# Kernel tuning notes

Measured on AMD Instinct MI355X. Metric: run time of the kernel, lower is better.

## Reference

```python
import jax, jax.numpy as jnp
import numpy as np

HIDDEN_DIM = 512
RADIUS = 128


def rel_pos_indexes(seq_len_q: int, seq_len_k: int, radius: int):
    # (i - j) clamped to [-radius, radius], shifted to [0, 2*radius]
    i = jnp.arange(seq_len_k)[None, :]   # [1, Sk]
    j = jnp.arange(seq_len_q)[:, None]   # [Sq, 1]
    return jnp.clip(i - j, -radius, radius) + radius  # [Sq, Sk] int


def setup_inputs() -> dict:
    key = jax.random.key(0)
    kq, kk, kv, ke = jax.random.split(key, 4)
    B, Sq, Sk, d = 4, 2048, 2048, HIDDEN_DIM
    Q = jax.random.normal(kq, (B, Sq, d), dtype=jnp.float32)
    K = jax.random.normal(kk, (B, Sk, d), dtype=jnp.float32)
    V = jax.random.normal(kv, (B, Sk, d), dtype=jnp.float32)
    # learned relative-position embedding table: (2R+1, d)
    rel_embeds = jax.random.normal(ke, (2 * RADIUS + 1, d), dtype=jnp.float32)
    return {"Q": Q, "K": K, "V": V, "rel_embeds": rel_embeds}


def reference(Q, K, V, rel_embeds):
    B, Sq, d = Q.shape
    Sk = K.shape[1]
    normalizer = jnp.asarray(d ** 0.5, dtype=Q.dtype)
    # content scores: [B, Sq, Sk]
    energy = jnp.einsum('bqd,bkd->bqk', Q, K)
    # relative scores: Q against the (2R+1) relative embeddings -> [B, Sq, 2R+1]
    Q_rel = jnp.einsum('bqd,rd->bqr', Q, rel_embeds)
    idx = rel_pos_indexes(Sq, Sk, RADIUS)  # [Sq, Sk]
    # gather along last dim per query row (same index map for every batch)
    rel_shift = jnp.take_along_axis(Q_rel, idx[None, :, :].repeat(B, axis=0), axis=2)
    energy = (energy + rel_shift) / normalizer
    attn = jax.nn.softmax(energy, axis=2)
    Z = jnp.einsum('bqk,bkd->bqd', attn, V)
    return attn, Z
```

## Files before the change

### kernel.cpp

```cpp
#include <hip/hip_runtime.h>

#define BATCH 4
#define SQL 2048
#define SKL 2048
#define DIM 512
#define NR 257
#define NRP 288
#define RAD 128

typedef __bf16 bf16x8 __attribute__((ext_vector_type(8)));
typedef float f32x4 __attribute__((ext_vector_type(4)));
typedef unsigned short u16;
typedef u16 u16x4 __attribute__((ext_vector_type(4)));
typedef u16 u16x8 __attribute__((ext_vector_type(8)));

__device__ inline u16 f2bf(float x) {
  union { float f; unsigned u; } v; v.f = x;
  unsigned r = v.u + 0x7FFF + ((v.u >> 16) & 1);
  return (u16)(r >> 16);
}

__device__ inline void glds16(const u16* g, const u16* l) {
  __builtin_amdgcn_global_load_lds(
      (const __attribute__((address_space(1))) void*)g,
      (__attribute__((address_space(3))) void*)l, 16, 0, 0);
}


__global__ void cvt_kernel(const f32x4* __restrict__ src, u16x4* __restrict__ dst, int n4) {
  int i = blockIdx.x * 256 + threadIdx.x;
  if (i >= n4) return;
  f32x4 f = src[i];
  u16x4 o;
#pragma unroll
  for (int e = 0; e < 4; e++) o[e] = f2bf(f[e]);
  dst[i] = o;
}

__global__ void cvt_rel_kernel(const float* __restrict__ rel, u16* __restrict__ relb) {
  int i = blockIdx.x * 256 + threadIdx.x;
  int r = i >> 9;
  relb[i] = (r < NR) ? f2bf(rel[i]) : (u16)0;
}

__global__ void transpose_v_kernel(const float* __restrict__ V, u16* __restrict__ Vt) {
  __shared__ float tile[32][33];
  int b = blockIdx.z;
  int k0 = blockIdx.x * 32, d0 = blockIdx.y * 32;
  int tx = threadIdx.x, ty = threadIdx.y;
#pragma unroll
  for (int r = 0; r < 4; r++)
    tile[ty + r * 8][tx] = V[((long)b * SKL + k0 + ty + r * 8) * DIM + d0 + tx];
  __syncthreads();
#pragma unroll
  for (int r = 0; r < 4; r++)
    Vt[((long)b * DIM + d0 + ty + r * 8) * SKL + k0 + tx] = f2bf(tile[tx][ty + r * 8]);
}

__global__ __launch_bounds__(256) void qrel_kernel(const u16* __restrict__ Qb,
                                                   const u16* __restrict__ relb,
                                                   float* __restrict__ Qrel) {
  int tid = threadIdx.x;
  int wave = tid >> 6, lane = tid & 63;
  int m0 = blockIdx.x * 64 + wave * 16;
  int j0 = blockIdx.y * 2;
  int fr = lane & 15, fk = (lane >> 4) * 8;
  f32x4 acc[2] = {};
  const u16* qrow = Qb + (long)(m0 + fr) * DIM + fk;
  const u16* r0 = relb + (long)(j0 * 16 + fr) * DIM + fk;
  const u16* r1 = r0 + 16 * DIM;
  for (int k0 = 0; k0 < DIM; k0 += 32) {
    bf16x8 a = *(const bf16x8*)(qrow + k0);
    bf16x8 b0 = *(const bf16x8*)(r0 + k0);
    bf16x8 b1 = *(const bf16x8*)(r1 + k0);
    acc[0] = __builtin_amdgcn_mfma_f32_16x16x32_bf16(a, b0, acc[0], 0, 0, 0);
    acc[1] = __builtin_amdgcn_mfma_f32_16x16x32_bf16(a, b1, acc[1], 0, 0, 0);
  }
  int cr = (lane >> 4) * 4, cc = lane & 15;
#pragma unroll
  for (int t = 0; t < 2; t++)
#pragma unroll
    for (int r = 0; r < 4; r++)
      Qrel[(long)(m0 + cr + r) * NRP + (j0 + t) * 16 + cc] = acc[t][r];
}

__global__ __launch_bounds__(256) void energy_kernel(const u16* __restrict__ Qb,
                                                     const u16* __restrict__ Kb,
                                                     const float* __restrict__ Qrel,
                                                     u16* __restrict__ S) {
  int b = blockIdx.z;
  int m0 = blockIdx.y * 128;
  int n0 = blockIdx.x * 128;
  const u16* A = Qb + (long)b * SQL * DIM;
  const u16* Bp = Kb + (long)b * SKL * DIM;
  __shared__ u16 As[128 * 32];
  __shared__ u16 Bs[128 * 32];
  int tid = threadIdx.x;
  int wave = tid >> 6, lane = tid & 63;
  int wm = (wave >> 1) * 64, wn = (wave & 1) * 64;
  int fr = lane & 15, fk = (lane >> 4) * 8;
  int srow = wave * 32 + (lane >> 2);
  int scol = (lane & 3) * 8;
  f32x4 acc[4][4] = {};
  for (int k0 = 0; k0 < DIM; k0 += 32) {
    __syncthreads();
    glds16(A + (long)(m0 + srow) * DIM + k0 + scol, As + (wave * 2 + 0) * 512);
    glds16(A + (long)(m0 + srow + 16) * DIM + k0 + scol, As + (wave * 2 + 1) * 512);
    glds16(Bp + (long)(n0 + srow) * DIM + k0 + scol, Bs + (wave * 2 + 0) * 512);
    glds16(Bp + (long)(n0 + srow + 16) * DIM + k0 + scol, Bs + (wave * 2 + 1) * 512);
    __syncthreads();
    bf16x8 af[4], bfr[4];
#pragma unroll
    for (int i = 0; i < 4; i++) af[i] = *(const bf16x8*)(As + (wm + i * 16 + fr) * 32 + fk);
#pragma unroll
    for (int j = 0; j < 4; j++) bfr[j] = *(const bf16x8*)(Bs + (wn + j * 16 + fr) * 32 + fk);
#pragma unroll
    for (int i = 0; i < 4; i++)
#pragma unroll
      for (int j = 0; j < 4; j++)
        acc[i][j] = __builtin_amdgcn_mfma_f32_16x16x32_bf16(af[i], bfr[j], acc[i][j], 0, 0, 0);
  }
  const float inv_norm = 0.04419417382415922f;
  int cr = (lane >> 4) * 4, cc = lane & 15;
#pragma unroll
  for (int i = 0; i < 4; i++) {
#pragma unroll
    for (int r = 0; r < 4; r++) {
      int q = m0 + wm + i * 16 + cr + r;
      const float* qrow = Qrel + ((long)b * SQL + q) * NRP;
      u16* sr = S + ((long)b * SQL + q) * SKL;
#pragma unroll
      for (int j = 0; j < 4; j++) {
        int k = n0 + wn + j * 16 + cc;
        int dlt = k - q;
        dlt = dlt < -RAD ? -RAD : (dlt > RAD ? RAD : dlt);
        sr[k] = f2bf((acc[i][j][r] + qrow[dlt + RAD]) * inv_norm);
      }
    }
  }
}

__global__ __launch_bounds__(256) void softmax_kernel(u16* __restrict__ S,
                                                      float* __restrict__ attn) {
  long row = blockIdx.x;
  u16* srow = S + row * SKL;
  float* arow = attn + row * SKL;
  int tid = threadIdx.x;
  int wave = tid >> 6, lane = tid & 63;
  bf16x8 v = *(const bf16x8*)(srow + tid * 8);
  float f[8];
#pragma unroll
  for (int e = 0; e < 8; e++) f[e] = (float)v[e];
  float m = -1e30f;
#pragma unroll
  for (int e = 0; e < 8; e++) m = fmaxf(m, f[e]);
  for (int o = 32; o > 0; o >>= 1) m = fmaxf(m, __shfl_xor(m, o));
  __shared__ float red[4];
  if (lane == 0) red[wave] = m;
  __syncthreads();
  m = fmaxf(fmaxf(red[0], red[1]), fmaxf(red[2], red[3]));
  __syncthreads();
  float s = 0.0f;
  float e8[8];
#pragma unroll
  for (int e = 0; e < 8; e++) { e8[e] = __expf(f[e] - m); s += e8[e]; }
  for (int o = 32; o > 0; o >>= 1) s += __shfl_xor(s, o);
  if (lane == 0) red[wave] = s;
  __syncthreads();
  s = red[0] + red[1] + red[2] + red[3];
  float inv = 1.0f / s;
  f32x4 o0, o1;
  u16x8 pb;
#pragma unroll
  for (int e = 0; e < 4; e++) {
    float p = e8[e] * inv;
    o0[e] = p; pb[e] = f2bf(p);
  }
#pragma unroll
  for (int e = 0; e < 4; e++) {
    float p = e8[e + 4] * inv;
    o1[e] = p; pb[e + 4] = f2bf(p);
  }
  *(f32x4*)(arow + tid * 8) = o0;
  *(f32x4*)(arow + tid * 8 + 4) = o1;
  *(u16x8*)(srow + tid * 8) = pb;
}

__global__ __launch_bounds__(256) void z_kernel(const u16* __restrict__ S,
                                                const u16* __restrict__ Vt,
                                                float* __restrict__ Z) {
  int b = blockIdx.z;
  int m0 = blockIdx.y * 64;
  int n0 = blockIdx.x * 128;
  const u16* A = S + (long)b * SQL * SKL;
  const u16* Bp = Vt + (long)b * DIM * SKL;
  __shared__ u16 As[64 * 32];
  __shared__ u16 Bs[128 * 32];
  int tid = threadIdx.x;
  int wave = tid >> 6, lane = tid & 63;
  int wm = (wave >> 1) * 32, wn = (wave & 1) * 64;
  int fr = lane & 15, fk = (lane >> 4) * 8;
  int srowA = wave * 16 + (lane >> 2);
  int srowB = wave * 32 + (lane >> 2);
  int scol = (lane & 3) * 8;
  f32x4 acc[2][4] = {};
  for (int k0 = 0; k0 < SKL; k0 += 32) {
    __syncthreads();
    glds16(A + (long)(m0 + srowA) * SKL + k0 + scol, As + wave * 512);
    glds16(Bp + (long)(n0 + srowB) * SKL + k0 + scol, Bs + (wave * 2 + 0) * 512);
    glds16(Bp + (long)(n0 + srowB + 16) * SKL + k0 + scol, Bs + (wave * 2 + 1) * 512);
    __syncthreads();
    bf16x8 af[2], bfr[4];
#pragma unroll
    for (int i = 0; i < 2; i++) af[i] = *(const bf16x8*)(As + (wm + i * 16 + fr) * 32 + fk);
#pragma unroll
    for (int j = 0; j < 4; j++) bfr[j] = *(const bf16x8*)(Bs + (wn + j * 16 + fr) * 32 + fk);
#pragma unroll
    for (int i = 0; i < 2; i++)
#pragma unroll
      for (int j = 0; j < 4; j++)
        acc[i][j] = __builtin_amdgcn_mfma_f32_16x16x32_bf16(af[i], bfr[j], acc[i][j], 0, 0, 0);
  }
  int cr = (lane >> 4) * 4, cc = lane & 15;
#pragma unroll
  for (int i = 0; i < 2; i++)
#pragma unroll
    for (int r = 0; r < 4; r++) {
      int q = m0 + wm + i * 16 + cr + r;
      float* zrow = Z + ((long)b * SQL + q) * DIM;
#pragma unroll
      for (int j = 0; j < 4; j++)
        zrow[n0 + wn + j * 16 + cc] = acc[i][j][r];
    }
}


extern "C" void kernel_launch(void* const* d_in, const int* in_sizes, int n_in,
                              void* d_out, int out_size, void* d_ws, size_t ws_size,
                              hipStream_t stream) {
  const float* Q = (const float*)d_in[0];
  const float* K = (const float*)d_in[1];
  const float* V = (const float*)d_in[2];
  const float* rel = (const float*)d_in[3];
  float* attn = (float*)d_out;
  float* Z = attn + (long)BATCH * SQL * SKL;

  char* ws = (char*)d_ws;
  u16* Qb   = (u16*)ws;
  u16* Kb   = (u16*)(ws + 8388608);
  u16* Vt   = (u16*)(ws + 16777216);
  u16* relb = (u16*)(ws + 25165824);
  float* Qrel = (float*)(ws + 25460736);
  u16* S    = (u16*)(ws + 34897920);

  cvt_kernel<<<4096, 256, 0, stream>>>((const f32x4*)Q, (u16x4*)Qb, 1048576);
  cvt_kernel<<<4096, 256, 0, stream>>>((const f32x4*)K, (u16x4*)Kb, 1048576);
  cvt_rel_kernel<<<576, 256, 0, stream>>>(rel, relb);
  transpose_v_kernel<<<dim3(64, 16, BATCH), dim3(32, 8), 0, stream>>>(V, Vt);
  qrel_kernel<<<dim3(128, 9), 256, 0, stream>>>(Qb, relb, Qrel);
  energy_kernel<<<dim3(16, 16, BATCH), 256, 0, stream>>>(Qb, Kb, Qrel, S);
  softmax_kernel<<<8192, 256, 0, stream>>>(S, attn);
  z_kernel<<<dim3(4, 32, BATCH), 256, 0, stream>>>(S, Vt, Z);
}
```

Measured before the change: 248.7 us.

## Fuse prep kernels and move relative-position bias add into softmax

Merges the Q/K conversion, V transpose, rel-embedding conversion and Q·rel GEMM into a single prep kernel, with the GEMM reading fp32 inputs directly. The relative bias gather moves out of the energy GEMM epilogue into the softmax kernel, which stages the row's scaled Qrel in LDS. This cuts launch overhead and the scattered global gathers in the energy epilogue, at the cost of a larger heterogeneous prep kernel and extra LDS work in softmax.

```diff
diff --git a/kernel.cpp b/kernel.cpp
--- a/kernel.cpp
+++ b/kernel.cpp
@@ -20,73 +20,86 @@
   return (u16)(r >> 16);
 }
 
+__device__ inline bf16x8 cvt8m(f32x4 lo, f32x4 hi, float m) {
+  u16x8 o;
+#pragma unroll
+  for (int e = 0; e < 4; e++) o[e] = f2bf(lo[e] * m);
+#pragma unroll
+  for (int e = 0; e < 4; e++) o[e + 4] = f2bf(hi[e] * m);
+  union { u16x8 u; bf16x8 b; } c; c.u = o; return c.b;
+}
+
 __device__ inline void glds16(const u16* g, const u16* l) {
   __builtin_amdgcn_global_load_lds(
       (const __attribute__((address_space(1))) void*)g,
       (__attribute__((address_space(3))) void*)l, 16, 0, 0);
 }
 
-
-__global__ void cvt_kernel(const f32x4* __restrict__ src, u16x4* __restrict__ dst, int n4) {
-  int i = blockIdx.x * 256 + threadIdx.x;
-  if (i >= n4) return;
-  f32x4 f = src[i];
-  u16x4 o;
-#pragma unroll
-  for (int e = 0; e < 4; e++) o[e] = f2bf(f[e]);
-  dst[i] = o;
-}
-
-__global__ void cvt_rel_kernel(const float* __restrict__ rel, u16* __restrict__ relb) {
-  int i = blockIdx.x * 256 + threadIdx.x;
-  int r = i >> 9;
-  relb[i] = (r < NR) ? f2bf(rel[i]) : (u16)0;
-}
-
-__global__ void transpose_v_kernel(const float* __restrict__ V, u16* __restrict__ Vt) {
+__global__ __launch_bounds__(256) void prep_kernel(const float* __restrict__ Q,
+                                                   const float* __restrict__ K,
+                                                   const float* __restrict__ V,
+                                                   const float* __restrict__ rel,
+                                                   u16x4* __restrict__ Qb,
+                                                   u16x4* __restrict__ Kb,
+                                                   u16* __restrict__ Vt,
+                                                   float* __restrict__ Qrel) {
   __shared__ float tile[32][33];
-  int b = blockIdx.z;
-  int k0 = blockIdx.x * 32, d0 = blockIdx.y * 32;
-  int tx = threadIdx.x, ty = threadIdx.y;
-#pragma unroll
-  for (int r = 0; r < 4; r++)
-    tile[ty + r * 8][tx] = V[((long)b * SKL + k0 + ty + r * 8) * DIM + d0 + tx];
-  __syncthreads();
-#pragma unroll
-  for (int r = 0; r < 4; r++)
-    Vt[((long)b * DIM + d0 + ty + r * 8) * SKL + k0 + tx] = f2bf(tile[tx][ty + r * 8]);
-}
-
-__global__ __launch_bounds__(256) void qrel_kernel(const u16* __restrict__ Qb,
-                                                   const u16* __restrict__ relb,
-                                                   float* __restrict__ Qrel) {
-  int tid = threadIdx.x;
-  int wave = tid >> 6, lane = tid & 63;
-  int m0 = blockIdx.x * 64 + wave * 16;
-  int j0 = blockIdx.y * 2;
-  int fr = lane & 15, fk = (lane >> 4) * 8;
-  f32x4 acc[2] = {};
-  const u16* qrow = Qb + (long)(m0 + fr) * DIM + fk;
-  const u16* r0 = relb + (long)(j0 * 16 + fr) * DIM + fk;
-  const u16* r1 = r0 + 16 * DIM;
-  for (int k0 = 0; k0 < DIM; k0 += 32) {
-    bf16x8 a = *(const bf16x8*)(qrow + k0);
-    bf16x8 b0 = *(const bf16x8*)(r0 + k0);
-    bf16x8 b1 = *(const bf16x8*)(r1 + k0);
-    acc[0] = __builtin_amdgcn_mfma_f32_16x16x32_bf16(a, b0, acc[0], 0, 0, 0);
-    acc[1] = __builtin_amdgcn_mfma_f32_16x16x32_bf16(a, b1, acc[1], 0, 0, 0);
-  }
-  int cr = (lane >> 4) * 4, cc = lane & 15;
-#pragma unroll
-  for (int t = 0; t < 2; t++)
+  int bid = blockIdx.x, tid = threadIdx.x;
+  if (bid < 8192) {
+    const f32x4* src = (bid < 4096) ? (const f32x4*)Q : (const f32x4*)K;
+    u16x4* dst = (bid < 4096) ? Qb : Kb;
+    int i = (bid & 4095) * 256 + tid;
+    f32x4 f = src[i];
+    u16x4 o;
+#pragma unroll
+    for (int e = 0; e < 4; e++) o[e] = f2bf(f[e]);
+    dst[i] = o;
+  } else if (bid < 12288) {
+    int t = bid - 8192;
+    int b = t >> 10, rem = t & 1023;
+    int k0 = (rem & 63) * 32, d0 = (rem >> 6) * 32;
+    int tx = tid & 31, ty = tid >> 5;
 #pragma unroll
     for (int r = 0; r < 4; r++)
-      Qrel[(long)(m0 + cr + r) * NRP + (j0 + t) * 16 + cc] = acc[t][r];
+      tile[ty + r * 8][tx] = V[((long)b * SKL + k0 + ty + r * 8) * DIM + d0 + tx];
+    __syncthreads();
+#pragma unroll
+    for (int r = 0; r < 4; r++)
+      Vt[((long)b * DIM + d0 + ty + r * 8) * SKL + k0 + tx] = f2bf(tile[tx][ty + r * 8]);
+  } else {
+    int t = bid - 12288;
+    int xb = t & 127, yb = t >> 7;
+    int wave = tid >> 6, lane = tid & 63;
+    int m0 = xb * 64 + wave * 16;
+    int j0 = yb * 2;
+    int fr = lane & 15, fk = (lane >> 4) * 8;
+    f32x4 acc[2] = {};
+    const float* qrow = Q + (long)(m0 + fr) * DIM + fk;
+    int r0r = j0 * 16 + fr, r1r = r0r + 16;
+    int r0c = r0r < NR ? r0r : NR - 1;
+    int r1c = r1r < NR ? r1r : NR - 1;
+    float g0 = r0r < NR ? 1.0f : 0.0f;
+    float g1 = r1r < NR ? 1.0f : 0.0f;
+    const float* r0p = rel + (long)r0c * DIM + fk;
+    const float* r1p = rel + (long)r1c * DIM + fk;
+    for (int k0 = 0; k0 < DIM; k0 += 32) {
+      bf16x8 a = cvt8m(*(const f32x4*)(qrow + k0), *(const f32x4*)(qrow + k0 + 4), 1.0f);
+      bf16x8 b0 = cvt8m(*(const f32x4*)(r0p + k0), *(const f32x4*)(r0p + k0 + 4), g0);
+      bf16x8 b1 = cvt8m(*(const f32x4*)(r1p + k0), *(const f32x4*)(r1p + k0 + 4), g1);
+      acc[0] = __builtin_amdgcn_mfma_f32_16x16x32_bf16(a, b0, acc[0], 0, 0, 0);
+      acc[1] = __builtin_amdgcn_mfma_f32_16x16x32_bf16(a, b1, acc[1], 0, 0, 0);
+    }
+    int cr = (lane >> 4) * 4, cc = lane & 15;
+#pragma unroll
+    for (int t2 = 0; t2 < 2; t2++)
+#pragma unroll
+      for (int r = 0; r < 4; r++)
+        Qrel[(long)(m0 + cr + r) * NRP + (j0 + t2) * 16 + cc] = acc[t2][r];
+  }
 }
 
 __global__ __launch_bounds__(256) void energy_kernel(const u16* __restrict__ Qb,
                                                      const u16* __restrict__ Kb,
-                                                     const float* __restrict__ Qrel,
                                                      u16* __restrict__ S) {
   int b = blockIdx.z;
   int m0 = blockIdx.y * 128;
@@ -127,35 +140,43 @@
 #pragma unroll
     for (int r = 0; r < 4; r++) {
       int q = m0 + wm + i * 16 + cr + r;
-      const float* qrow = Qrel + ((long)b * SQL + q) * NRP;
       u16* sr = S + ((long)b * SQL + q) * SKL;
 #pragma unroll
-      for (int j = 0; j < 4; j++) {
-        int k = n0 + wn + j * 16 + cc;
-        int dlt = k - q;
-        dlt = dlt < -RAD ? -RAD : (dlt > RAD ? RAD : dlt);
-        sr[k] = f2bf((acc[i][j][r] + qrow[dlt + RAD]) * inv_norm);
-      }
+      for (int j = 0; j < 4; j++)
+        sr[n0 + wn + j * 16 + cc] = f2bf(acc[i][j][r] * inv_norm);
     }
   }
 }
 
 __global__ __launch_bounds__(256) void softmax_kernel(u16* __restrict__ S,
+                                                      const float* __restrict__ Qrel,
                                                       float* __restrict__ attn) {
   long row = blockIdx.x;
+  int q = (int)(row & (SQL - 1));
   u16* srow = S + row * SKL;
   float* arow = attn + row * SKL;
   int tid = threadIdx.x;
   int wave = tid >> 6, lane = tid & 63;
+  __shared__ float qlds[NR];
+  __shared__ float red[4];
+  const float inv_norm = 0.04419417382415922f;
+  const float* qr = Qrel + row * NRP;
+  qlds[tid] = qr[tid] * inv_norm;
+  if (tid == 0) qlds[256] = qr[256] * inv_norm;
   bf16x8 v = *(const bf16x8*)(srow + tid * 8);
+  __syncthreads();
   float f[8];
-#pragma unroll
-  for (int e = 0; e < 8; e++) f[e] = (float)v[e];
+  int kb = tid * 8 - q + RAD;
+#pragma unroll
+  for (int e = 0; e < 8; e++) {
+    int idx = kb + e;
+    idx = idx < 0 ? 0 : (idx > 2 * RAD ? 2 * RAD : idx);
+    f[e] = (float)v[e] + qlds[idx];
+  }
   float m = -1e30f;
 #pragma unroll
   for (int e = 0; e < 8; e++) m = fmaxf(m, f[e]);
   for (int o = 32; o > 0; o >>= 1) m = fmaxf(m, __shfl_xor(m, o));
-  __shared__ float red[4];
   if (lane == 0) red[wave] = m;
   __syncthreads();
   m = fmaxf(fmaxf(red[0], red[1]), fmaxf(red[2], red[3]));
@@ -249,16 +270,11 @@
   u16* Qb   = (u16*)ws;
   u16* Kb   = (u16*)(ws + 8388608);
   u16* Vt   = (u16*)(ws + 16777216);
-  u16* relb = (u16*)(ws + 25165824);
-  float* Qrel = (float*)(ws + 25460736);
-  u16* S    = (u16*)(ws + 34897920);
-
-  cvt_kernel<<<4096, 256, 0, stream>>>((const f32x4*)Q, (u16x4*)Qb, 1048576);
-  cvt_kernel<<<4096, 256, 0, stream>>>((const f32x4*)K, (u16x4*)Kb, 1048576);
-  cvt_rel_kernel<<<576, 256, 0, stream>>>(rel, relb);
-  transpose_v_kernel<<<dim3(64, 16, BATCH), dim3(32, 8), 0, stream>>>(V, Vt);
-  qrel_kernel<<<dim3(128, 9), 256, 0, stream>>>(Qb, relb, Qrel);
-  energy_kernel<<<dim3(16, 16, BATCH), 256, 0, stream>>>(Qb, Kb, Qrel, S);
-  softmax_kernel<<<8192, 256, 0, stream>>>(S, attn);
+  float* Qrel = (float*)(ws + 25165824);
+  u16* S    = (u16*)(ws + 34603008);
+
+  prep_kernel<<<13440, 256, 0, stream>>>(Q, K, V, rel, (u16x4*)Qb, (u16x4*)Kb, Vt, Qrel);
+  energy_kernel<<<dim3(16, 16, BATCH), 256, 0, stream>>>(Qb, Kb, S);
+  softmax_kernel<<<8192, 256, 0, stream>>>(S, Qrel, attn);
   z_kernel<<<dim3(4, 32, BATCH), 256, 0, stream>>>(S, Vt, Z);
 }
```

Measured after the change: 280.6 us. 12.8% more time.
